# Optimization experiments

Hardware: AMD Instinct MI355X
Metric: run time of the kernel (lower is better)

The kernel has to match this reference:

```python
import jax, jax.numpy as jnp
import numpy as np

N_NODES = 20000
N_EDGES = 320000
D_IN = 128      # input_dim == width_encoder == width_decoder == output_dim
D_HID = 256     # width
BN_EPS = 1e-5


def _lin_init(key, out_dim, in_dim, bias=True):
    kw, kb = jax.random.split(key)
    s = 1.0 / np.sqrt(in_dim)
    W = jax.random.uniform(kw, (out_dim, in_dim), jnp.float32, -s, s)
    if bias:
        b = jax.random.uniform(kb, (out_dim,), jnp.float32, -s, s)
        return W, b
    return W


def setup_inputs() -> dict:
    key = jax.random.key(0)
    ks = jax.random.split(key, 16)
    x = jax.random.normal(ks[0], (N_NODES, D_IN), jnp.float32)
    edge_index = jax.random.randint(ks[1], (2, N_EDGES), 0, N_NODES, jnp.int64)
    enc_W, enc_b = _lin_init(ks[2], D_IN, D_IN)
    # SAGEConv layers: lin_l (aggregated neighbors, with bias), lin_r (root, no bias)
    Wl0, bl0 = _lin_init(ks[3], D_HID, D_IN)
    Wr0 = _lin_init(ks[4], D_HID, D_IN, bias=False)
    Wl1, bl1 = _lin_init(ks[5], D_HID, D_HID)
    Wr1 = _lin_init(ks[6], D_HID, D_HID, bias=False)
    Wl2, bl2 = _lin_init(ks[7], D_HID, D_HID)
    Wr2 = _lin_init(ks[8], D_HID, D_HID, bias=False)
    Wl3, bl3 = _lin_init(ks[9], D_IN, D_HID)
    Wr3 = _lin_init(ks[10], D_IN, D_HID, bias=False)
    # BatchNorm affine params (3 layers on D_HID)
    g0 = jnp.ones((D_HID,), jnp.float32); b0 = jnp.zeros((D_HID,), jnp.float32)
    g1 = jnp.ones((D_HID,), jnp.float32); b1 = jnp.zeros((D_HID,), jnp.float32)
    g2 = jnp.ones((D_HID,), jnp.float32); b2 = jnp.zeros((D_HID,), jnp.float32)
    dec_W, dec_b = _lin_init(ks[11], D_IN, D_IN)
    return dict(x=x, edge_index=edge_index, enc_W=enc_W, enc_b=enc_b,
                Wl0=Wl0, bl0=bl0, Wr0=Wr0, Wl1=Wl1, bl1=bl1, Wr1=Wr1,
                Wl2=Wl2, bl2=bl2, Wr2=Wr2, Wl3=Wl3, bl3=bl3, Wr3=Wr3,
                g0=g0, b0=b0, g1=g1, b1=b1, g2=g2, b2=b2,
                dec_W=dec_W, dec_b=dec_b)


def _sage(z, src, dst, Wl, bl, Wr, n_nodes):
    # mean-aggregate neighbor messages: scatter-mean of z[src] onto dst
    msg = z[src]                                            # [E, d]
    agg = jax.ops.segment_sum(msg, dst, num_segments=n_nodes)
    cnt = jax.ops.segment_sum(jnp.ones((src.shape[0], 1), z.dtype), dst,
                              num_segments=n_nodes)
    mean = agg / jnp.maximum(cnt, 1.0)                      # [N, d]
    return mean @ Wl.T + bl + z @ Wr.T


def _bn(z, gamma, beta):
    # BatchNorm1d(track_running_stats=False): always batch stats, biased var
    m = jnp.mean(z, axis=0)
    v = jnp.var(z, axis=0)
    return (z - m) * jax.lax.rsqrt(v + BN_EPS) * gamma + beta


def reference(x, edge_index, enc_W, enc_b,
              Wl0, bl0, Wr0, Wl1, bl1, Wr1, Wl2, bl2, Wr2, Wl3, bl3, Wr3,
              g0, b0, g1, b1, g2, b2, dec_W, dec_b):
    src, dst = edge_index[0], edge_index[1]
    n = x.shape[0]
    z = x @ enc_W.T + enc_b                                  # encoder (single Linear)
    z = jax.nn.relu(_bn(_sage(z, src, dst, Wl0, bl0, Wr0, n), g0, b0))
    z = jax.nn.relu(_bn(_sage(z, src, dst, Wl1, bl1, Wr1, n), g1, b1))
    z = jax.nn.relu(_bn(_sage(z, src, dst, Wl2, bl2, Wr2, n), g2, b2))
    z = _sage(z, src, dst, Wl3, bl3, Wr3, n)
    z = z @ dec_W.T + dec_b                                  # decoder (single Linear)
    return z
```

## Files before the change

### kernel.cpp

```cpp
#include <hip/hip_runtime.h>

#define N_NODES 20000
#define N_EDGES 320000
#define NPAD    20032
#define BN_EPS  1e-5f
#define NBLK    79

using bf16x8 = __attribute__((ext_vector_type(8))) short;
using f32x4  = __attribute__((ext_vector_type(4))) float;

__device__ __forceinline__ float bf2f(ushort u) {
  union { unsigned i; float f; } t; t.i = ((unsigned)u) << 16; return t.f;
}
__device__ __forceinline__ ushort f2bf(float f) {
  unsigned x = __float_as_uint(f);
  return (ushort)((x + 0x7fffu + ((x >> 16) & 1u)) >> 16);
}

__global__ void k_deg(const int* __restrict__ dst, int* __restrict__ deg) {
  int t = blockIdx.x * blockDim.x + threadIdx.x;
  if (t < N_EDGES) { unsigned d = (unsigned)dst[t]; if (d < N_NODES) atomicAdd(&deg[d], 1); }
}

__global__ void k_scanA(const int* __restrict__ deg, int* __restrict__ part,
                        int* __restrict__ bsum) {
  __shared__ int buf[256];
  int i = blockIdx.x * 256 + threadIdx.x;
  int v = (i < N_NODES) ? deg[i] : 0;
  buf[threadIdx.x] = v;
  __syncthreads();
  #pragma unroll
  for (int s = 1; s < 256; s <<= 1) {
    int t = (threadIdx.x >= s) ? buf[threadIdx.x - s] : 0;
    __syncthreads();
    buf[threadIdx.x] += t;
    __syncthreads();
  }
  if (i < N_NODES) part[i] = buf[threadIdx.x];
  if (threadIdx.x == 255) bsum[blockIdx.x] = buf[255];
}

__global__ void k_scanB(int* __restrict__ bsum) {
  __shared__ int buf[128];
  int v = (threadIdx.x < NBLK) ? bsum[threadIdx.x] : 0;
  buf[threadIdx.x] = v;
  __syncthreads();
  #pragma unroll
  for (int s = 1; s < 128; s <<= 1) {
    int t = (threadIdx.x >= s) ? buf[threadIdx.x - s] : 0;
    __syncthreads();
    buf[threadIdx.x] += t;
    __syncthreads();
  }
  if (threadIdx.x < NBLK) bsum[threadIdx.x] = buf[threadIdx.x];
}

__global__ void k_scanC(const int* __restrict__ deg, const int* __restrict__ part,
                        const int* __restrict__ bsum, int* __restrict__ rowptr,
                        float* __restrict__ inv) {
  int i = blockIdx.x * 256 + threadIdx.x;
  if (i >= N_NODES) return;
  int off = blockIdx.x ? bsum[blockIdx.x - 1] : 0;
  rowptr[i + 1] = off + part[i];
  if (i == 0) rowptr[0] = 0;
  inv[i] = 1.0f / (float)max(deg[i], 1);
}

__global__ void k_fill(const int* __restrict__ src, const int* __restrict__ dst,
                       int* __restrict__ cursor, int* __restrict__ col) {
  int e = blockIdx.x * blockDim.x + threadIdx.x;
  if (e >= N_EDGES) return;
  unsigned d = (unsigned)dst[e];
  if (d >= N_NODES) return;
  int p = atomicAdd(&cursor[d], 1);
  col[p] = src[e];
}

__global__ void k_cvtw(const float* s0, const float* s1, const float* s2,
                       const float* s3, const float* s4, const float* s5,
                       const float* s6, const float* s7, const float* s8,
                       const float* s9, ushort* __restrict__ dst) {
  int t = blockIdx.x * blockDim.x + threadIdx.x;
  int e = t * 4;
  if (e >= 425984) return;
  const float* s; int off;
  if      (e < 16384)  { s = s0; off = e; }
  else if (e < 49152)  { s = s1; off = e - 16384; }
  else if (e < 81920)  { s = s2; off = e - 49152; }
  else if (e < 147456) { s = s3; off = e - 81920; }
  else if (e < 212992) { s = s4; off = e - 147456; }
  else if (e < 278528) { s = s5; off = e - 212992; }
  else if (e < 344064) { s = s6; off = e - 278528; }
  else if (e < 376832) { s = s7; off = e - 344064; }
  else if (e < 409600) { s = s8; off = e - 376832; }
  else                 { s = s9; off = e - 409600; }
  float4 v = *(const float4*)(s + off);
  dst[e + 0] = f2bf(v.x); dst[e + 1] = f2bf(v.y);
  dst[e + 2] = f2bf(v.z); dst[e + 3] = f2bf(v.w);
}

template <int DIM, bool BN>
__global__ __launch_bounds__(256) void k_gather(
    const ushort* __restrict__ z, const int* __restrict__ rowptr,
    const int* __restrict__ col, const float* __restrict__ inv,
    const float* __restrict__ bnp, ushort* __restrict__ mean) {
  int node = blockIdx.x * 4 + (threadIdx.x >> 6);
  if (node >= N_NODES) return;
  int lane = threadIdx.x & 63;
  constexpr int V = DIM / 64;
  float sc[V], sh[V];
  if constexpr (BN) {
    #pragma unroll
    for (int k = 0; k < V; ++k) { sc[k] = bnp[lane * V + k]; sh[k] = bnp[256 + lane * V + k]; }
  }
  float acc[V] = {};
  int r0 = rowptr[node], r1 = rowptr[node + 1];
  #pragma unroll 2
  for (int j = r0; j < r1; ++j) {
    int s = col[j];
    const ushort* zp = z + (size_t)s * DIM + lane * V;
    if constexpr (V == 4) {
      ushort4 v = *(const ushort4*)zp;
      float f0 = bf2f(v.x), f1 = bf2f(v.y), f2 = bf2f(v.z), f3 = bf2f(v.w);
      if constexpr (BN) {
        f0 = fmaxf(f0 * sc[0] + sh[0], 0.f); f1 = fmaxf(f1 * sc[1] + sh[1], 0.f);
        f2 = fmaxf(f2 * sc[2] + sh[2], 0.f); f3 = fmaxf(f3 * sc[3] + sh[3], 0.f);
      }
      acc[0] += f0; acc[1] += f1; acc[2] += f2; acc[3] += f3;
    } else {
      ushort2 v = *(const ushort2*)zp;
      float f0 = bf2f(v.x), f1 = bf2f(v.y);
      if constexpr (BN) {
        f0 = fmaxf(f0 * sc[0] + sh[0], 0.f); f1 = fmaxf(f1 * sc[1] + sh[1], 0.f);
      }
      acc[0] += f0; acc[1] += f1;
    }
  }
  float iv = inv[node];
  ushort* mp = mean + (size_t)node * DIM + lane * V;
  #pragma unroll
  for (int k = 0; k < V; ++k) mp[k] = f2bf(acc[k] * iv);
}

template <int DIN>
__device__ __forceinline__ void stage_w(const ushort* __restrict__ Wsrc, char* Wt) {
  constexpr int LOGR = (DIN == 256) ? 9 : 8;
  const char* g = (const char*)Wsrc;
  #pragma unroll
  for (int i = 0; i < (64 * DIN * 2) / 4096; ++i) {
    int p = i * 4096 + threadIdx.x * 16;
    int row = p >> LOGR;
    bf16x8 v = *(const bf16x8*)(g + p);
    *(bf16x8*)(Wt + (p ^ ((row & 7) << 4))) = v;
  }
}

template <bool AF32, bool BN, int DIN>
__device__ __forceinline__ void load_a(const void* __restrict__ A,
                                       const float* __restrict__ bnp,
                                       int arow, int lb, bf16x8* af) {
  #pragma unroll
  for (int kk = 0; kk < DIN / 32; ++kk) {
    if constexpr (AF32) {
      const float* ap = (const float*)A + (size_t)arow * DIN + kk * 32 + lb * 8;
      float4 u = *(const float4*)ap;
      float4 v = *(const float4*)(ap + 4);
      bf16x8 a;
      a[0] = (short)f2bf(u.x); a[1] = (short)f2bf(u.y);
      a[2] = (short)f2bf(u.z); a[3] = (short)f2bf(u.w);
      a[4] = (short)f2bf(v.x); a[5] = (short)f2bf(v.y);
      a[6] = (short)f2bf(v.z); a[7] = (short)f2bf(v.w);
      af[kk] = a;
    } else {
      bf16x8 r = *(const bf16x8*)((const ushort*)A + (size_t)arow * DIN + kk * 32 + lb * 8);
      if constexpr (BN) {
        int c0 = kk * 32 + lb * 8;
        float4 s0 = *(const float4*)(bnp + c0);
        float4 s1 = *(const float4*)(bnp + c0 + 4);
        float4 h0 = *(const float4*)(bnp + 256 + c0);
        float4 h1 = *(const float4*)(bnp + 256 + c0 + 4);
        r[0] = (short)f2bf(fmaxf(bf2f((ushort)r[0]) * s0.x + h0.x, 0.f));
        r[1] = (short)f2bf(fmaxf(bf2f((ushort)r[1]) * s0.y + h0.y, 0.f));
        r[2] = (short)f2bf(fmaxf(bf2f((ushort)r[2]) * s0.z + h0.z, 0.f));
        r[3] = (short)f2bf(fmaxf(bf2f((ushort)r[3]) * s0.w + h0.w, 0.f));
        r[4] = (short)f2bf(fmaxf(bf2f((ushort)r[4]) * s1.x + h1.x, 0.f));
        r[5] = (short)f2bf(fmaxf(bf2f((ushort)r[5]) * s1.y + h1.y, 0.f));
        r[6] = (short)f2bf(fmaxf(bf2f((ushort)r[6]) * s1.z + h1.z, 0.f));
        r[7] = (short)f2bf(fmaxf(bf2f((ushort)r[7]) * s1.w + h1.w, 0.f));
      }
      af[kk] = r;
    }
  }
}

template <int DIN>
__device__ __forceinline__ void compute(const bf16x8* af, const char* Wt,
                                        int la, int lb, f32x4* acc) {
  constexpr int LOGR = (DIN == 256) ? 9 : 8;
  #pragma unroll
  for (int kk = 0; kk < DIN / 32; ++kk) {
    #pragma unroll
    for (int nf = 0; nf < 4; ++nf) {
      int r = nf * 16 + la;
      int ad = (r << LOGR) + (kk * 32 + lb * 8) * 2;
      ad ^= ((r & 7) << 4);
      bf16x8 b = *(const bf16x8*)(Wt + ad);
      acc[nf] = __builtin_amdgcn_mfma_f32_16x16x32_bf16(af[kk], b, acc[nf], 0, 0, 0);
    }
  }
}

template <bool AF32, bool CF32, int DIN, int DOUT, bool DUAL, bool BNA2, bool STATS,
          bool SAMEW>
__global__ __launch_bounds__(256) void k_gemm(
    const void* __restrict__ A1v, const ushort* __restrict__ W1,
    const void* __restrict__ A2v, const ushort* __restrict__ W2,
    const float* __restrict__ bias, const float* __restrict__ bnp,
    float* __restrict__ stats, void* __restrict__ Cv, int Mstore)
{
  __shared__ __align__(16) char Wt[64 * DIN * 2];
  __shared__ float sbuf[64], qbuf[64];
  int lane = threadIdx.x & 63, wid = threadIdx.x >> 6;
  int la = lane & 15, lb = lane >> 4;
  int rowBase = blockIdx.y * 64 + wid * 16;
  int colBase = blockIdx.x * 64;
  int arow = rowBase + la; if (arow >= N_NODES) arow = N_NODES - 1;

  if constexpr (STATS) {
    if (threadIdx.x < 64) { sbuf[threadIdx.x] = 0.f; qbuf[threadIdx.x] = 0.f; }
  }

  f32x4 acc[4];
  #pragma unroll
  for (int i = 0; i < 4; ++i) acc[i] = {0.f, 0.f, 0.f, 0.f};

  bf16x8 af[DIN / 32];
  load_a<AF32, false, DIN>(A1v, nullptr, arow, lb, af);
  stage_w<DIN>(W1 + (size_t)colBase * DIN, Wt);
  __syncthreads();
  compute<DIN>(af, Wt, la, lb, acc);

  if constexpr (DUAL) {
    if constexpr (SAMEW) {
      load_a<false, BNA2, DIN>(A2v, bnp, arow, lb, af);
      compute<DIN>(af, Wt, la, lb, acc);
    } else {
      __syncthreads();
      load_a<false, BNA2, DIN>(A2v, bnp, arow, lb, af);
      stage_w<DIN>(W2 + (size_t)colBase * DIN, Wt);
      __syncthreads();
      compute<DIN>(af, Wt, la, lb, acc);
    }
  }

  float colsum[4] = {}, colsq[4] = {};
  #pragma unroll
  for (int nf = 0; nf < 4; ++nf) {
    int col = colBase + nf * 16 + la;
    float bv = bias ? bias[col] : 0.0f;
    #pragma unroll
    for (int i = 0; i < 4; ++i) {
      int row = rowBase + lb * 4 + i;
      float o = acc[nf][i] + bv;
      if (row < Mstore) {
        if constexpr (CF32) ((float*)Cv)[(size_t)row * DOUT + col] = o;
        else                ((ushort*)Cv)[(size_t)row * DOUT + col] = f2bf(o);
      }
      if constexpr (STATS) {
        if (row < N_NODES) { colsum[nf] += o; colsq[nf] += o * o; }
      }
    }
  }

  if constexpr (STATS) {
    #pragma unroll
    for (int nf = 0; nf < 4; ++nf) {
      float sv = colsum[nf], qv = colsq[nf];
      sv += __shfl_xor(sv, 16); qv += __shfl_xor(qv, 16);
      sv += __shfl_xor(sv, 32); qv += __shfl_xor(qv, 32);
      if (lb == 0) { atomicAdd(&sbuf[nf * 16 + la], sv); atomicAdd(&qbuf[nf * 16 + la], qv); }
    }
    __syncthreads();
    if (threadIdx.x < 64)        atomicAdd(&stats[colBase + threadIdx.x], sbuf[threadIdx.x]);
    else if (threadIdx.x < 128)  atomicAdd(&stats[256 + colBase + threadIdx.x - 64], qbuf[threadIdx.x - 64]);
  }
}

__global__ __launch_bounds__(256) void k_gemm_pq(
    const ushort* __restrict__ z, const ushort* __restrict__ Wl,
    const ushort* __restrict__ Wr, const float* __restrict__ bl,
    const float* __restrict__ bnp, ushort* __restrict__ P, ushort* __restrict__ Q)
{
  constexpr int DIN = 256, DOUT = 128;
  __shared__ __align__(16) char Wt[64 * DIN * 2];
  int lane = threadIdx.x & 63, wid = threadIdx.x >> 6;
  int la = lane & 15, lb = lane >> 4;
  int rowBase = blockIdx.y * 64 + wid * 16;
  int colBase = blockIdx.x * 64;
  int arow = rowBase + la; if (arow >= N_NODES) arow = N_NODES - 1;

  bf16x8 af[DIN / 32];
  load_a<false, true, DIN>(z, bnp, arow, lb, af);
  stage_w<DIN>(Wl + (size_t)colBase * DIN, Wt);
  __syncthreads();

  f32x4 acc[4];
  #pragma unroll
  for (int i = 0; i < 4; ++i) acc[i] = {0.f, 0.f, 0.f, 0.f};
  compute<DIN>(af, Wt, la, lb, acc);
  #pragma unroll
  for (int nf = 0; nf < 4; ++nf) {
    int col = colBase + nf * 16 + la;
    #pragma unroll
    for (int i = 0; i < 4; ++i) {
      int row = rowBase + lb * 4 + i;
      if (row < N_NODES) P[(size_t)row * DOUT + col] = f2bf(acc[nf][i]);
    }
  }

  __syncthreads();
  stage_w<DIN>(Wr + (size_t)colBase * DIN, Wt);
  __syncthreads();
  #pragma unroll
  for (int i = 0; i < 4; ++i) acc[i] = {0.f, 0.f, 0.f, 0.f};
  compute<DIN>(af, Wt, la, lb, acc);
  #pragma unroll
  for (int nf = 0; nf < 4; ++nf) {
    int col = colBase + nf * 16 + la;
    float bv = bl[col];
    #pragma unroll
    for (int i = 0; i < 4; ++i) {
      int row = rowBase + lb * 4 + i;
      if (row < N_NODES) Q[(size_t)row * DOUT + col] = f2bf(acc[nf][i] + bv);
    }
  }
}

__global__ void k_bnprep(const float* __restrict__ stats, const float* __restrict__ gamma,
                         const float* __restrict__ beta, float* __restrict__ bnp) {
  int c = threadIdx.x;
  float m = stats[c] * (1.0f / N_NODES);
  float var = stats[256 + c] * (1.0f / N_NODES) - m * m;
  float rs = rsqrtf(var + BN_EPS);
  float sc = rs * gamma[c];
  bnp[c] = sc;
  bnp[256 + c] = beta[c] - m * sc;
}

extern "C" void kernel_launch(void* const* d_in, const int* in_sizes, int n_in,
                              void* d_out, int out_size, void* d_ws, size_t ws_size,
                              hipStream_t stream) {
  const float* x    = (const float*)d_in[0];
  const int*   ei   = (const int*)d_in[1];
  const float* encW = (const float*)d_in[2];
  const float* encb = (const float*)d_in[3];
  const float* Wl0  = (const float*)d_in[4];
  const float* bl0  = (const float*)d_in[5];
  const float* Wr0  = (const float*)d_in[6];
  const float* Wl1  = (const float*)d_in[7];
  const float* bl1  = (const float*)d_in[8];
  const float* Wr1  = (const float*)d_in[9];
  const float* Wl2  = (const float*)d_in[10];
  const float* bl2  = (const float*)d_in[11];
  const float* Wr2  = (const float*)d_in[12];
  const float* Wl3  = (const float*)d_in[13];
  const float* bl3  = (const float*)d_in[14];
  const float* Wr3  = (const float*)d_in[15];
  const float* g0   = (const float*)d_in[16];
  const float* b0   = (const float*)d_in[17];
  const float* g1   = (const float*)d_in[18];
  const float* b1   = (const float*)d_in[19];
  const float* g2   = (const float*)d_in[20];
  const float* b2   = (const float*)d_in[21];
  const float* decW = (const float*)d_in[22];
  const float* decb = (const float*)d_in[23];

  const int* src = ei;
  const int* dst = ei + N_EDGES;

  char* ws = (char*)d_ws;
  size_t off = 0;
  auto alloc = [&](size_t bytes) { char* p = ws + off; off += (bytes + 255) & ~255ull; return p; };
  ushort* bufA   = (ushort*)alloc((size_t)NPAD * 256 * 2);
  ushort* bufB   = (ushort*)alloc((size_t)NPAD * 256 * 2);
  ushort* mean   = (ushort*)alloc((size_t)NPAD * 256 * 2);
  int*    deg    = (int*)   alloc((size_t)N_NODES * 4);
  int*    part   = (int*)   alloc((size_t)N_NODES * 4);
  int*    bsum   = (int*)   alloc(128 * 4);
  int*    rowptr = (int*)   alloc((size_t)(N_NODES + 1) * 4);
  int*    cursor = (int*)   alloc((size_t)N_NODES * 4);
  int*    colidx = (int*)   alloc((size_t)N_EDGES * 4);
  float*  inv    = (float*) alloc((size_t)N_NODES * 4);
  float*  stats  = (float*) alloc(3 * 512 * 4);
  float*  bnp    = (float*) alloc(3 * 512 * 4);
  ushort* wpool  = (ushort*)alloc(425984 * 2);

  float* stats0 = stats, *stats1 = stats + 512, *stats2 = stats + 1024;
  float* bnp0 = bnp, *bnp1 = bnp + 512, *bnp2 = bnp + 1024;

  const ushort* wEnc = wpool;
  const ushort* wL0  = wpool + 16384;
  const ushort* wR0  = wpool + 49152;
  const ushort* wL1  = wpool + 81920;
  const ushort* wR1  = wpool + 147456;
  const ushort* wL2  = wpool + 212992;
  const ushort* wR2  = wpool + 278528;
  const ushort* wL3  = wpool + 344064;
  const ushort* wR3  = wpool + 376832;
  const ushort* wDec = wpool + 409600;

  hipMemsetAsync(deg, 0, (size_t)N_NODES * 4, stream);
  hipMemsetAsync(stats, 0, 3 * 512 * 4, stream);
  k_deg<<<(N_EDGES + 255) / 256, 256, 0, stream>>>(dst, deg);
  k_scanA<<<NBLK, 256, 0, stream>>>(deg, part, bsum);
  k_scanB<<<1, 128, 0, stream>>>(bsum);
  k_scanC<<<NBLK, 256, 0, stream>>>(deg, part, bsum, rowptr, inv);
  hipMemcpyAsync(cursor, rowptr, (size_t)N_NODES * 4, hipMemcpyDeviceToDevice, stream);
  k_fill<<<(N_EDGES + 255) / 256, 256, 0, stream>>>(src, dst, cursor, colidx);

  k_cvtw<<<(106496 + 255) / 256, 256, 0, stream>>>(encW, Wl0, Wr0, Wl1, Wr1, Wl2, Wr2,
                                                   Wl3, Wr3, decW, wpool);

  const int GGRID = NPAD / 64;
  const int NGB = (N_NODES + 3) / 4;

  k_gemm<true, false, 128, 128, false, false, false, false>
      <<<dim3(2, GGRID), 256, 0, stream>>>(
      x, wEnc, nullptr, nullptr, encb, nullptr, nullptr, bufA, N_NODES);

  k_gather<128, false><<<NGB, 256, 0, stream>>>(bufA, rowptr, colidx, inv, nullptr, mean);
  k_gemm<false, false, 128, 256, true, false, true, false>
      <<<dim3(4, GGRID), 256, 0, stream>>>(
      mean, wL0, bufA, wR0, bl0, nullptr, stats0, bufB, N_NODES);
  k_bnprep<<<1, 256, 0, stream>>>(stats0, g0, b0, bnp0);

  k_gather<256, true><<<NGB, 256, 0, stream>>>(bufB, rowptr, colidx, inv, bnp0, mean);
  k_gemm<false, false, 256, 256, true, true, true, false>
      <<<dim3(4, GGRID), 256, 0, stream>>>(
      mean, wL1, bufB, wR1, bl1, bnp0, stats1, bufA, N_NODES);
  k_bnprep<<<1, 256, 0, stream>>>(stats1, g1, b1, bnp1);

  k_gather<256, true><<<NGB, 256, 0, stream>>>(bufA, rowptr, colidx, inv, bnp1, mean);
  k_gemm<false, false, 256, 256, true, true, true, false>
      <<<dim3(4, GGRID), 256, 0, stream>>>(
      mean, wL2, bufA, wR2, bl2, bnp1, stats2, bufB, N_NODES);
  k_bnprep<<<1, 256, 0, stream>>>(stats2, g2, b2, bnp2);

  ushort* P = mean;
  ushort* Q = mean + (size_t)NPAD * 128;
  k_gemm_pq<<<dim3(2, GGRID), 256, 0, stream>>>(bufB, wL3, wR3, bl3, bnp2, P, Q);

  k_gather<128, false><<<NGB, 256, 0, stream>>>(P, rowptr, colidx, inv, nullptr, bufA);

  k_gemm<false, true, 128, 128, true, false, false, true>
      <<<dim3(2, GGRID), 256, 0, stream>>>(
      bufA, wDec, Q, nullptr, decb, nullptr, nullptr, (float*)d_out, N_NODES);
}
```

Measured before the change: 275.5 us.

## Fuse preprocessing launches and gather multiple neighbors per wavefront with 16-byte loads

Weight conversion and degree counting now share one kernel, and one memset clears both deg and stats. The separate block-sum scan kernel and the device-to-device cursor copy are gone: scanC sums block totals serially per block and writes cursor directly. The gather kernel now splits each wavefront into lane groups that load different neighbors with 8-wide bf16 vector loads and combine partial sums via shuffles. This cuts launch count and improves memory parallelism in the gather, in exchange for extra shuffle reductions and a serial prefix loop in scanC.

```diff
diff --git a/kernel.cpp b/kernel.cpp
--- a/kernel.cpp
+++ b/kernel.cpp
@@ -5,6 +5,7 @@
 #define NPAD    20032
 #define BN_EPS  1e-5f
 #define NBLK    79
+#define CVTB    416
 
 using bf16x8 = __attribute__((ext_vector_type(8))) short;
 using f32x4  = __attribute__((ext_vector_type(4))) float;
@@ -17,9 +18,36 @@
   return (ushort)((x + 0x7fffu + ((x >> 16) & 1u)) >> 16);
 }
 
-__global__ void k_deg(const int* __restrict__ dst, int* __restrict__ deg) {
-  int t = blockIdx.x * blockDim.x + threadIdx.x;
-  if (t < N_EDGES) { unsigned d = (unsigned)dst[t]; if (d < N_NODES) atomicAdd(&deg[d], 1); }
+__global__ void k_prep(const float* s0, const float* s1, const float* s2,
+                       const float* s3, const float* s4, const float* s5,
+                       const float* s6, const float* s7, const float* s8,
+                       const float* s9, ushort* __restrict__ wdst,
+                       const int* __restrict__ edst, int* __restrict__ deg) {
+  int b = blockIdx.x;
+  if (b < CVTB) {
+    int e = (b * 256 + threadIdx.x) * 4;
+    if (e >= 425984) return;
+    const float* s; int off;
+    if      (e < 16384)  { s = s0; off = e; }
+    else if (e < 49152)  { s = s1; off = e - 16384; }
+    else if (e < 81920)  { s = s2; off = e - 49152; }
+    else if (e < 147456) { s = s3; off = e - 81920; }
+    else if (e < 212992) { s = s4; off = e - 147456; }
+    else if (e < 278528) { s = s5; off = e - 212992; }
+    else if (e < 344064) { s = s6; off = e - 278528; }
+    else if (e < 376832) { s = s7; off = e - 344064; }
+    else if (e < 409600) { s = s8; off = e - 376832; }
+    else                 { s = s9; off = e - 409600; }
+    float4 v = *(const float4*)(s + off);
+    wdst[e + 0] = f2bf(v.x); wdst[e + 1] = f2bf(v.y);
+    wdst[e + 2] = f2bf(v.z); wdst[e + 3] = f2bf(v.w);
+  } else {
+    int t = (b - CVTB) * 256 + threadIdx.x;
+    if (t < N_EDGES) {
+      unsigned d = (unsigned)edst[t];
+      if (d < N_NODES) atomicAdd(&deg[d], 1);
+    }
+  }
 }
 
 __global__ void k_scanA(const int* __restrict__ deg, int* __restrict__ part,
@@ -40,30 +68,24 @@
   if (threadIdx.x == 255) bsum[blockIdx.x] = buf[255];
 }
 
-__global__ void k_scanB(int* __restrict__ bsum) {
-  __shared__ int buf[128];
-  int v = (threadIdx.x < NBLK) ? bsum[threadIdx.x] : 0;
-  buf[threadIdx.x] = v;
-  __syncthreads();
-  #pragma unroll
-  for (int s = 1; s < 128; s <<= 1) {
-    int t = (threadIdx.x >= s) ? buf[threadIdx.x - s] : 0;
-    __syncthreads();
-    buf[threadIdx.x] += t;
-    __syncthreads();
-  }
-  if (threadIdx.x < NBLK) bsum[threadIdx.x] = buf[threadIdx.x];
-}
-
 __global__ void k_scanC(const int* __restrict__ deg, const int* __restrict__ part,
                         const int* __restrict__ bsum, int* __restrict__ rowptr,
-                        float* __restrict__ inv) {
+                        int* __restrict__ cursor, float* __restrict__ inv) {
+  __shared__ int soff;
+  if (threadIdx.x == 0) {
+    int o = 0;
+    for (int b = 0; b < blockIdx.x; ++b) o += bsum[b];
+    soff = o;
+  }
+  __syncthreads();
   int i = blockIdx.x * 256 + threadIdx.x;
   if (i >= N_NODES) return;
-  int off = blockIdx.x ? bsum[blockIdx.x - 1] : 0;
-  rowptr[i + 1] = off + part[i];
+  int r1 = soff + part[i];
+  int d = deg[i];
+  rowptr[i + 1] = r1;
+  cursor[i] = r1 - d;
   if (i == 0) rowptr[0] = 0;
-  inv[i] = 1.0f / (float)max(deg[i], 1);
+  inv[i] = 1.0f / (float)max(d, 1);
 }
 
 __global__ void k_fill(const int* __restrict__ src, const int* __restrict__ dst,
@@ -76,70 +98,54 @@
   col[p] = src[e];
 }
 
-__global__ void k_cvtw(const float* s0, const float* s1, const float* s2,
-                       const float* s3, const float* s4, const float* s5,
-                       const float* s6, const float* s7, const float* s8,
-                       const float* s9, ushort* __restrict__ dst) {
-  int t = blockIdx.x * blockDim.x + threadIdx.x;
-  int e = t * 4;
-  if (e >= 425984) return;
-  const float* s; int off;
-  if      (e < 16384)  { s = s0; off = e; }
-  else if (e < 49152)  { s = s1; off = e - 16384; }
-  else if (e < 81920)  { s = s2; off = e - 49152; }
-  else if (e < 147456) { s = s3; off = e - 81920; }
-  else if (e < 212992) { s = s4; off = e - 147456; }
-  else if (e < 278528) { s = s5; off = e - 212992; }
-  else if (e < 344064) { s = s6; off = e - 278528; }
-  else if (e < 376832) { s = s7; off = e - 344064; }
-  else if (e < 409600) { s = s8; off = e - 376832; }
-  else                 { s = s9; off = e - 409600; }
-  float4 v = *(const float4*)(s + off);
-  dst[e + 0] = f2bf(v.x); dst[e + 1] = f2bf(v.y);
-  dst[e + 2] = f2bf(v.z); dst[e + 3] = f2bf(v.w);
-}
-
 template <int DIM, bool BN>
 __global__ __launch_bounds__(256) void k_gather(
     const ushort* __restrict__ z, const int* __restrict__ rowptr,
     const int* __restrict__ col, const float* __restrict__ inv,
     const float* __restrict__ bnp, ushort* __restrict__ mean) {
+  constexpr int LPR = DIM / 8;
+  constexpr int NPW = 64 / LPR;
   int node = blockIdx.x * 4 + (threadIdx.x >> 6);
   if (node >= N_NODES) return;
   int lane = threadIdx.x & 63;
-  constexpr int V = DIM / 64;
-  float sc[V], sh[V];
+  int grp = lane / LPR;
+  int sub = lane % LPR;
+  float sc[8], sh[8];
   if constexpr (BN) {
     #pragma unroll
-    for (int k = 0; k < V; ++k) { sc[k] = bnp[lane * V + k]; sh[k] = bnp[256 + lane * V + k]; }
-  }
-  float acc[V] = {};
+    for (int k = 0; k < 8; ++k) {
+      sc[k] = bnp[sub * 8 + k];
+      sh[k] = bnp[256 + sub * 8 + k];
+    }
+  }
+  float acc[8] = {};
   int r0 = rowptr[node], r1 = rowptr[node + 1];
   #pragma unroll 2
-  for (int j = r0; j < r1; ++j) {
-    int s = col[j];
-    const ushort* zp = z + (size_t)s * DIM + lane * V;
-    if constexpr (V == 4) {
-      ushort4 v = *(const ushort4*)zp;
-      float f0 = bf2f(v.x), f1 = bf2f(v.y), f2 = bf2f(v.z), f3 = bf2f(v.w);
-      if constexpr (BN) {
-        f0 = fmaxf(f0 * sc[0] + sh[0], 0.f); f1 = fmaxf(f1 * sc[1] + sh[1], 0.f);
-        f2 = fmaxf(f2 * sc[2] + sh[2], 0.f); f3 = fmaxf(f3 * sc[3] + sh[3], 0.f);
-      }
-      acc[0] += f0; acc[1] += f1; acc[2] += f2; acc[3] += f3;
-    } else {
-      ushort2 v = *(const ushort2*)zp;
-      float f0 = bf2f(v.x), f1 = bf2f(v.y);
-      if constexpr (BN) {
-        f0 = fmaxf(f0 * sc[0] + sh[0], 0.f); f1 = fmaxf(f1 * sc[1] + sh[1], 0.f);
-      }
-      acc[0] += f0; acc[1] += f1;
-    }
-  }
-  float iv = inv[node];
-  ushort* mp = mean + (size_t)node * DIM + lane * V;
-  #pragma unroll
-  for (int k = 0; k < V; ++k) mp[k] = f2bf(acc[k] * iv);
+  for (int j = r0; j < r1; j += NPW) {
+    int jj = j + grp;
+    bool val = jj < r1;
+    int nb = val ? col[jj] : 0;
+    bf16x8 v = *(const bf16x8*)(z + (size_t)nb * DIM + sub * 8);
+    float w = val ? 1.f : 0.f;
+    #pragma unroll
+    for (int k = 0; k < 8; ++k) {
+      float f = bf2f((ushort)v[k]);
+      if constexpr (BN) f = fmaxf(f * sc[k] + sh[k], 0.f);
+      acc[k] += f * w;
+    }
+  }
+  #pragma unroll
+  for (int k = 0; k < 8; ++k) {
+    if constexpr (NPW == 4) acc[k] += __shfl_xor(acc[k], 16);
+    acc[k] += __shfl_xor(acc[k], 32);
+  }
+  if (grp == 0) {
+    float iv = inv[node];
+    bf16x8 o;
+    #pragma unroll
+    for (int k = 0; k < 8; ++k) o[k] = (short)f2bf(acc[k] * iv);
+    *(bf16x8*)(mean + (size_t)node * DIM + sub * 8) = o;
+  }
 }
 
 template <int DIN>
@@ -385,13 +391,13 @@
   ushort* bufB   = (ushort*)alloc((size_t)NPAD * 256 * 2);
   ushort* mean   = (ushort*)alloc((size_t)NPAD * 256 * 2);
   int*    deg    = (int*)   alloc((size_t)N_NODES * 4);
+  float*  stats  = (float*) alloc(3 * 512 * 4);
   int*    part   = (int*)   alloc((size_t)N_NODES * 4);
   int*    bsum   = (int*)   alloc(128 * 4);
   int*    rowptr = (int*)   alloc((size_t)(N_NODES + 1) * 4);
   int*    cursor = (int*)   alloc((size_t)N_NODES * 4);
   int*    colidx = (int*)   alloc((size_t)N_EDGES * 4);
   float*  inv    = (float*) alloc((size_t)N_NODES * 4);
-  float*  stats  = (float*) alloc(3 * 512 * 4);
   float*  bnp    = (float*) alloc(3 * 512 * 4);
   ushort* wpool  = (ushort*)alloc(425984 * 2);
 
@@ -409,17 +415,13 @@
   const ushort* wR3  = wpool + 376832;
   const ushort* wDec = wpool + 409600;
 
-  hipMemsetAsync(deg, 0, (size_t)N_NODES * 4, stream);
-  hipMemsetAsync(stats, 0, 3 * 512 * 4, stream);
-  k_deg<<<(N_EDGES + 255) / 256, 256, 0, stream>>>(dst, deg);
+  size_t degPad = ((size_t)N_NODES * 4 + 255) & ~255ull;
+  hipMemsetAsync(deg, 0, degPad + 3 * 512 * 4, stream);
+  k_prep<<<CVTB + (N_EDGES + 255) / 256, 256, 0, stream>>>(
+      encW, Wl0, Wr0, Wl1, Wr1, Wl2, Wr2, Wl3, Wr3, decW, wpool, dst, deg);
   k_scanA<<<NBLK, 256, 0, stream>>>(deg, part, bsum);
-  k_scanB<<<1, 128, 0, stream>>>(bsum);
-  k_scanC<<<NBLK, 256, 0, stream>>>(deg, part, bsum, rowptr, inv);
-  hipMemcpyAsync(cursor, rowptr, (size_t)N_NODES * 4, hipMemcpyDeviceToDevice, stream);
+  k_scanC<<<NBLK, 256, 0, stream>>>(deg, part, bsum, rowptr, cursor, inv);
   k_fill<<<(N_EDGES + 255) / 256, 256, 0, stream>>>(src, dst, cursor, colidx);
-
-  k_cvtw<<<(106496 + 255) / 256, 256, 0, stream>>>(encW, Wl0, Wr0, Wl1, Wr1, Wl2, Wr2,
-                                                   Wl3, Wr3, decW, wpool);
 
   const int GGRID = NPAD / 64;
   const int NGB = (N_NODES + 3) / 4;
```

New measurement: 249.0 us. 9.6% less time.
